# Kernel optimization log

Measured on AMD Instinct MI355X. Metric: run time of the kernel, lower is better.

Reference implementation:

```python
import jax, jax.numpy as jnp
import numpy as np

BSZ, SEQ, D, NHEAD, NLAYER, DFF, NQ = 4, 48, 256, 2, 2, 2048, 512
LN_EPS = 1e-5
NEG = jnp.float32(-1e30)


def _layernorm(x, w, b):
    m = jnp.mean(x, axis=-1, keepdims=True)
    v = jnp.mean((x - m) ** 2, axis=-1, keepdims=True)
    return (x - m) / jnp.sqrt(v + LN_EPS) * w + b


def _span_max(x):
    # Cumulative span max: span[b,s,e] = max(x[b,s:e+1]) for e>=s, else 0.
    B, S, H = x.shape
    padded = jnp.concatenate([x, jnp.full((B, S, H), NEG, x.dtype)], axis=1)  # [B,2S,H]

    def step(tmp, i):
        shifted = jax.lax.dynamic_slice(padded, (0, i, 0), (B, S, H))  # x shifted left by i, padded with -inf
        tmp = jnp.maximum(tmp, shifted)  # tmp[b,s] = max(x[b,s:s+i+1])
        return tmp, tmp

    _, ys = jax.lax.scan(step, jnp.full((B, S, H), NEG, x.dtype), jnp.arange(S))
    # ys: [width, B, start, H]; span[b,s,e] = ys[e-s, b, s]
    si = jnp.arange(S)[:, None]
    ei = jnp.arange(S)[None, :]
    w = jnp.clip(ei - si, 0, S - 1)
    span = ys[w, :, jnp.broadcast_to(si, (S, S))]  # [S_start, S_end, B, H]
    span = jnp.where((ei >= si)[:, :, None, None], span, 0.0)
    return span.transpose(2, 0, 1, 3)  # [B,S,S,H]


def _mha(x, wi, bi, wo, bo, kpm):
    # x: [B,T,D]; kpm: [B,T] bool, True = masked key
    B, T, Dm = x.shape
    hd = Dm // NHEAD
    qkv = x @ wi.T + bi
    q, k, v = jnp.split(qkv, 3, axis=-1)
    rs = lambda a: a.reshape(B, T, NHEAD, hd).transpose(0, 2, 1, 3)
    q, k, v = rs(q), rs(k), rs(v)
    scores = jnp.einsum('bhqd,bhkd->bhqk', q, k) * (1.0 / np.sqrt(hd))
    scores = jnp.where(kpm[:, None, None, :], -1e9, scores)
    p = jax.nn.softmax(scores, axis=-1)
    o = jnp.einsum('bhqk,bhkd->bhqd', p, v).transpose(0, 2, 1, 3).reshape(B, T, Dm)
    return o @ wo.T + bo


def _encoder(x, kpm, iw, ib, ow, ob, l1w, l1b, l2w, l2b, f1w, f1b, f2w, f2b, fw, fb):
    # Post-norm torch TransformerEncoder (eval mode, relu, no dropout)
    for l in range(NLAYER):
        a = _mha(x, iw[l], ib[l], ow[l], ob[l], kpm)
        x = _layernorm(x + a, l1w[l], l1b[l])
        f = jax.nn.relu(x @ f1w[l].T + f1b[l]) @ f2w[l].T + f2b[l]
        x = _layernorm(x + f, l2w[l], l2b[l])
    return _layernorm(x, fw, fb)


def _forward(enc, iw, ib, ow, ob, l1w, l1b, l2w, l2b, f1w, f1b, f2w, f2b, fw, fb, s1, e1, qb, s2, e2):
    span = _span_max(enc)  # [B,S,S,D]
    idx = jnp.arange(SEQ)
    kpm2d = idx[None, :] < idx[:, None]  # [start,end]: True where end < start
    kpm = jnp.broadcast_to(kpm2d.reshape(1, SEQ * SEQ), (BSZ, SEQ * SEQ))
    out = _encoder(span.reshape(BSZ, SEQ * SEQ, D), kpm, iw, ib, ow, ob, l1w, l1b, l2w, l2b, f1w, f1b, f2w, f2b, fw, fb)
    out = out.reshape(BSZ, SEQ, SEQ, D)
    res1 = out[qb, s1, e1]
    res2 = out[qb, s2, e2]
    return res1, res2


def setup_inputs() -> dict:
    key = jax.random.key(0)
    ks = jax.random.split(key, 16)
    sc = 0.02
    enc = jax.random.normal(ks[0], (BSZ, SEQ, D), jnp.float32)
    inp = {
        'encoded_input': enc,
        'in_proj_w': jax.random.normal(ks[1], (NLAYER, 3 * D, D), jnp.float32) * sc,
        'in_proj_b': jnp.zeros((NLAYER, 3 * D), jnp.float32),
        'out_proj_w': jax.random.normal(ks[2], (NLAYER, D, D), jnp.float32) * sc,
        'out_proj_b': jnp.zeros((NLAYER, D), jnp.float32),
        'ln1_w': jnp.ones((NLAYER, D), jnp.float32),
        'ln1_b': jnp.zeros((NLAYER, D), jnp.float32),
        'ln2_w': jnp.ones((NLAYER, D), jnp.float32),
        'ln2_b': jnp.zeros((NLAYER, D), jnp.float32),
        'ff1_w': jax.random.normal(ks[3], (NLAYER, DFF, D), jnp.float32) * sc,
        'ff1_b': jnp.zeros((NLAYER, DFF), jnp.float32),
        'ff2_w': jax.random.normal(ks[4], (NLAYER, D, DFF), jnp.float32) * sc,
        'ff2_b': jnp.zeros((NLAYER, D), jnp.float32),
        'fln_w': jnp.ones((D,), jnp.float32),
        'fln_b': jnp.zeros((D,), jnp.float32),
    }
    s1 = jax.random.randint(ks[5], (NQ,), 0, SEQ)
    e1 = jnp.minimum(s1 + jax.random.randint(ks[6], (NQ,), 0, SEQ), SEQ - 1)
    s2 = jax.random.randint(ks[7], (NQ,), 0, SEQ)
    e2 = jnp.minimum(s2 + jax.random.randint(ks[8], (NQ,), 0, SEQ), SEQ - 1)
    inp['start_ids_1'] = s1
    inp['end_ids_1'] = e1
    inp['query_batch_idx'] = jax.random.randint(ks[9], (NQ,), 0, BSZ)
    inp['start_ids_2'] = s2
    inp['end_ids_2'] = e2
    return inp


def reference(encoded_input, in_proj_w, in_proj_b, out_proj_w, out_proj_b, ln1_w, ln1_b, ln2_w, ln2_b, ff1_w, ff1_b, ff2_w, ff2_b, fln_w, fln_b, start_ids_1, end_ids_1, query_batch_idx, start_ids_2, end_ids_2):
    return _forward(encoded_input, in_proj_w, in_proj_b, out_proj_w, out_proj_b, ln1_w, ln1_b, ln2_w, ln2_b, ff1_w, ff1_b, ff2_w, ff2_b, fln_w, fln_b, start_ids_1, end_ids_1, query_batch_idx, start_ids_2, end_ids_2)
```

## Files before the change

### kernel.cpp

```cpp
#include <hip/hip_runtime.h>
#include <hip/hip_bf16.h>

#define BSZ 4
#define SEQ 48
#define DMODEL 256
#define NHEAD 2
#define HD 128
#define NLAYERS 2
#define DFF_C 2048
#define NQ_C 512
#define NV 1176
#define NTOT (BSZ * NV)
#define NVP 1216
#define KSPLIT 5
#define SCALE 0.088388347648318447f

typedef unsigned short u16;
typedef __attribute__((ext_vector_type(8))) short bf16x8;
typedef __attribute__((ext_vector_type(4))) float f32x4;

__device__ inline u16 f2b(float f) {
    __hip_bfloat16 h = __float2bfloat16(f);
    return *reinterpret_cast<u16*>(&h);
}
__device__ inline void storeval(float* p, float v) { *p = v; }
__device__ inline void storeval(u16* p, float v) { *p = f2b(v); }

__global__ __launch_bounds__(256) void span_kernel(const float* __restrict__ enc,
                                                   float* __restrict__ X,
                                                   u16* __restrict__ Xb) {
    int i = blockIdx.x, b = blockIdx.y, h = threadIdx.x;
    int tb = i * SEQ - (i * (i - 1)) / 2 - i;
    float run = -1e30f;
    for (int j = i; j < SEQ; ++j) {
        run = fmaxf(run, enc[((size_t)b * SEQ + j) * DMODEL + h]);
        size_t idx = ((size_t)b * NV + tb + j) * DMODEL + h;
        X[idx] = run;
        Xb[idx] = f2b(run);
    }
}

__global__ __launch_bounds__(256) void castall_kernel(
    const float* __restrict__ iw, const float* __restrict__ ow,
    const float* __restrict__ f1w, const float* __restrict__ f2w,
    u16* __restrict__ iwb, u16* __restrict__ owb,
    u16* __restrict__ f1wb, u16* __restrict__ f2wb) {
    int i = blockIdx.x * 256 + threadIdx.x;
    const float* src;
    u16* dst;
    int off;
    if (i < 98304)       { src = iw;  dst = iwb;  off = i; }
    else if (i < 131072) { src = ow;  dst = owb;  off = i - 98304; }
    else if (i < 393216) { src = f1w; dst = f1wb; off = i - 131072; }
    else                 { src = f2w; dst = f2wb; off = i - 393216; }
    float4 v = *(const float4*)(src + (size_t)off * 4);
    *(ushort4*)(dst + (size_t)off * 4) =
        make_ushort4(f2b(v.x), f2b(v.y), f2b(v.z), f2b(v.w));
}

template <typename OutT, bool RELU, bool ATOMIC>
__global__ __launch_bounds__(256) void mm_kernel(
    const u16* __restrict__ A, const u16* __restrict__ W,
    const float* __restrict__ bias, const float* __restrict__ Res,
    OutT* __restrict__ C, int N, int K, int lda, int ldw, int ldc,
    float alpha, int WV, int KC) {
    __shared__ u16 As[64][40];
    __shared__ u16 Ws[64][40];
    const float4 fz = make_float4(0.f, 0.f, 0.f, 0.f);
    int ks = blockIdx.z;
    int kb = ks * KC, ke = min(K, kb + KC);
    int p0 = blockIdx.x * 64, n0 = blockIdx.y * 64;
    int tid = threadIdx.x, lane = tid & 63, w = tid >> 6;
    int col_l = lane & 15, quad = lane >> 4;
    f32x4 acc[4] = {};
    for (int k0 = kb; k0 < ke; k0 += 32) {
        int r = tid >> 2, seg = (tid & 3) * 8;
        {
            int gn = n0 + r;
            float4 av = fz;
            if (gn < N) av = *(const float4*)(A + (size_t)gn * lda + k0 + seg);
            *(float4*)&As[r][seg] = av;
        }
        {
            int gp = p0 + r;
            float4 wv = fz;
            if (gp < WV) wv = *(const float4*)(W + (size_t)gp * ldw + k0 + seg);
            *(float4*)&Ws[r][seg] = wv;
        }
        __syncthreads();
        bf16x8 a = *(const bf16x8*)&As[w * 16 + col_l][quad * 8];
#pragma unroll
        for (int c = 0; c < 4; ++c) {
            bf16x8 b = *(const bf16x8*)&Ws[c * 16 + col_l][quad * 8];
            acc[c] = __builtin_amdgcn_mfma_f32_16x16x32_bf16(a, b, acc[c], 0, 0, 0);
        }
        __syncthreads();
    }
#pragma unroll
    for (int c = 0; c < 4; ++c) {
        int col = p0 + c * 16 + col_l;
        float bv = bias ? bias[col] : 0.f;
#pragma unroll
        for (int reg = 0; reg < 4; ++reg) {
            int row = n0 + w * 16 + quad * 4 + reg;
            if (row < N) {
                float v = acc[c][reg] * alpha + bv;
                if (Res) v += Res[(size_t)row * ldc + col];
                if (RELU) v = fmaxf(v, 0.f);
                if (ATOMIC) {
                    unsafeAtomicAdd((float*)&C[(size_t)row * ldc + col], v);
                } else {
                    storeval(&C[(size_t)row * ldc + col], v);
                }
            }
        }
    }
}

__global__ __launch_bounds__(256) void vtrans_kernel(const u16* __restrict__ QKVb,
                                                     u16* __restrict__ VT) {
    __shared__ u16 T[64][66];
    const float4 fz = make_float4(0.f, 0.f, 0.f, 0.f);
    int kt = blockIdx.x, dt = blockIdx.y, bh = blockIdx.z;
    int b = bh >> 1, h = bh & 1;
    size_t rb = (size_t)b * NV;
    int tid = threadIdx.x;
    {
        int r = tid >> 2, cs = (tid & 3) * 16;
        int key = kt * 64 + r;
        float4 v0 = fz, v1 = fz;
        if (key < NV) {
            const u16* vp = QKVb + (rb + key) * 768 + 2 * DMODEL + h * HD + dt * 64 + cs;
            v0 = *(const float4*)vp;
            v1 = *(const float4*)(vp + 8);
        }
        *(float4*)&T[r][cs] = v0;
        *(float4*)&T[r][cs + 8] = v1;
    }
    __syncthreads();
    {
        int dl = tid >> 2, ks2 = (tid & 3) * 16;
        u16 tmp[16];
#pragma unroll
        for (int j = 0; j < 16; ++j) tmp[j] = T[ks2 + j][dl];
        u16* dst = VT + ((size_t)bh * HD + dt * 64 + dl) * NVP + kt * 64 + ks2;
        *(float4*)dst = *(float4*)&tmp[0];
        *(float4*)(dst + 8) = *(float4*)&tmp[8];
    }
}

__global__ __launch_bounds__(256) void flash_kernel(const u16* __restrict__ QKVb,
                                                    const u16* __restrict__ VT,
                                                    float* __restrict__ Opart,
                                                    float* __restrict__ ML) {
    __shared__ u16 Ks[64][136];
    __shared__ u16 Vt[128][72];
    __shared__ u16 Ps[4][16][72];
    const float4 fz = make_float4(0.f, 0.f, 0.f, 0.f);
    int tid = threadIdx.x, lane = tid & 63, w = tid >> 6;
    int col_l = lane & 15, quad = lane >> 4;
    int bh = blockIdx.y, b = bh >> 1, h = bh & 1;
    int ks = blockIdx.z;
    int t0 = ks * 4, tcnt = min(4, 19 - t0);
    size_t rb = (size_t)b * NV;
    int q0 = blockIdx.x * 64, wq0 = q0 + w * 16;

    float4 qv[4];
    {
        int qrow = wq0 + col_l;
        if (qrow < NV) {
            const u16* qp = QKVb + (rb + qrow) * 768 + h * HD + quad * 8;
#pragma unroll
            for (int kf = 0; kf < 4; ++kf) qv[kf] = *(const float4*)(qp + kf * 32);
        } else {
#pragma unroll
            for (int kf = 0; kf < 4; ++kf) qv[kf] = fz;
        }
    }

    f32x4 oacc[8] = {};
    float m_run[4], l_run[4];
#pragma unroll
    for (int r = 0; r < 4; ++r) { m_run[r] = -1e30f; l_run[r] = 0.f; }

    for (int it = 0; it < tcnt; ++it) {
        int kt = (t0 + it) * 64;
        {
            int r = tid >> 2, seg = (tid & 3) * 32;
            int key = kt + r;
            const u16* kp = QKVb + (rb + key) * 768 + DMODEL + h * HD + seg;
#pragma unroll
            for (int t4 = 0; t4 < 4; ++t4) {
                float4 v = fz;
                if (key < NV) v = *(const float4*)(kp + t4 * 8);
                *(float4*)&Ks[r][seg + t4 * 8] = v;
            }
        }
        {
            int d = tid >> 1, half = (tid & 1) * 32;
            const u16* vp = VT + ((size_t)bh * HD + d) * NVP + kt + half;
#pragma unroll
            for (int t4 = 0; t4 < 4; ++t4)
                *(float4*)&Vt[d][half + t4 * 8] = *(const float4*)(vp + t4 * 8);
        }
        __syncthreads();

        f32x4 s[4] = {};
#pragma unroll
        for (int c = 0; c < 4; ++c)
#pragma unroll
            for (int kf = 0; kf < 4; ++kf) {
                bf16x8 kfr = *(const bf16x8*)&Ks[c * 16 + col_l][kf * 32 + quad * 8];
                s[c] = __builtin_amdgcn_mfma_f32_16x16x32_bf16(
                    *(const bf16x8*)&qv[kf], kfr, s[c], 0, 0, 0);
            }

        float pv[4][4];
#pragma unroll
        for (int c = 0; c < 4; ++c) {
            bool kvalid = (kt + c * 16 + col_l) < NV;
#pragma unroll
            for (int r = 0; r < 4; ++r)
                pv[c][r] = kvalid ? s[c][r] * SCALE : -1e30f;
        }
        float al[4];
#pragma unroll
        for (int r = 0; r < 4; ++r) {
            float mx = fmaxf(fmaxf(pv[0][r], pv[1][r]), fmaxf(pv[2][r], pv[3][r]));
#pragma unroll
            for (int off = 1; off < 16; off <<= 1)
                mx = fmaxf(mx, __shfl_xor(mx, off));
            float mn = fmaxf(m_run[r], mx);
            al[r] = __expf(m_run[r] - mn);
            m_run[r] = mn;
            float sum = 0.f;
#pragma unroll
            for (int c = 0; c < 4; ++c) {
                float p = __expf(pv[c][r] - mn);
                pv[c][r] = p;
                sum += p;
            }
#pragma unroll
            for (int off = 1; off < 16; off <<= 1) sum += __shfl_xor(sum, off);
            l_run[r] = l_run[r] * al[r] + sum;
        }
#pragma unroll
        for (int ct = 0; ct < 8; ++ct)
#pragma unroll
            for (int r = 0; r < 4; ++r) oacc[ct][r] *= al[r];

#pragma unroll
        for (int c = 0; c < 4; ++c)
#pragma unroll
            for (int r = 0; r < 4; ++r)
                Ps[w][quad * 4 + r][c * 16 + col_l] = f2b(pv[c][r]);
        bf16x8 pf0 = *(const bf16x8*)&Ps[w][col_l][quad * 8];
        bf16x8 pf1 = *(const bf16x8*)&Ps[w][col_l][32 + quad * 8];
#pragma unroll
        for (int ct = 0; ct < 8; ++ct) {
            bf16x8 v0 = *(const bf16x8*)&Vt[ct * 16 + col_l][quad * 8];
            bf16x8 v1 = *(const bf16x8*)&Vt[ct * 16 + col_l][32 + quad * 8];
            oacc[ct] = __builtin_amdgcn_mfma_f32_16x16x32_bf16(pf0, v0, oacc[ct], 0, 0, 0);
            oacc[ct] = __builtin_amdgcn_mfma_f32_16x16x32_bf16(pf1, v1, oacc[ct], 0, 0, 0);
        }
        __syncthreads();
    }

    size_t slab = (size_t)(ks * 8 + bh) * NVP;
#pragma unroll
    for (int ct = 0; ct < 8; ++ct)
#pragma unroll
        for (int r = 0; r < 4; ++r) {
            int row = wq0 + quad * 4 + r;
            Opart[(slab + row) * HD + ct * 16 + col_l] = oacc[ct][r];
        }
    if (col_l == 0) {
#pragma unroll
        for (int r = 0; r < 4; ++r) {
            int row = wq0 + quad * 4 + r;
            ML[(slab + row) * 2 + 0] = m_run[r];
            ML[(slab + row) * 2 + 1] = l_run[r];
        }
    }
}

__global__ __launch_bounds__(256) void comb_kernel(const float* __restrict__ Opart,
                                                   const float* __restrict__ ML,
                                                   u16* __restrict__ Obuf) {
    int bh = blockIdx.y, b = bh >> 1, h = bh & 1;
    int tid = threadIdx.x;
    int row = blockIdx.x * 2 + (tid >> 7);
    int d = tid & 127;
    if (row >= NV) return;
    float m[KSPLIT], l[KSPLIT];
#pragma unroll
    for (int i = 0; i < KSPLIT; ++i) {
        size_t mb = ((size_t)(i * 8 + bh) * NVP + row) * 2;
        m[i] = ML[mb];
        l[i] = ML[mb + 1];
    }
    float M = m[0];
#pragma unroll
    for (int i = 1; i < KSPLIT; ++i) M = fmaxf(M, m[i]);
    float wsum = 0.f, o = 0.f;
#pragma unroll
    for (int i = 0; i < KSPLIT; ++i) {
        float wi = __expf(m[i] - M);
        wsum += l[i] * wi;
        o += Opart[((size_t)(i * 8 + bh) * NVP + row) * HD + d] * wi;
    }
    Obuf[((size_t)b * NV + row) * DMODEL + h * HD + d] = f2b(o / wsum);
}

__global__ __launch_bounds__(256) void ln_kernel(const float* __restrict__ Xin,
                                                 const float* __restrict__ Res,
                                                 const float* __restrict__ w,
                                                 const float* __restrict__ bb,
                                                 float* __restrict__ Y,
                                                 u16* __restrict__ Yb,
                                                 const float* __restrict__ fb2,
                                                 float* __restrict__ A2out) {
    int r = blockIdx.x, d = threadIdx.x;
    size_t idx = (size_t)r * DMODEL + d;
    float v = Xin[idx];
    if (Res) v += Res[idx];
    float s1 = v, s2 = v * v;
#pragma unroll
    for (int off = 32; off > 0; off >>= 1) {
        s1 += __shfl_down(s1, off);
        s2 += __shfl_down(s2, off);
    }
    __shared__ float ps1[4], ps2[4];
    int wid = d >> 6, lane = d & 63;
    if (lane == 0) { ps1[wid] = s1; ps2[wid] = s2; }
    __syncthreads();
    if (d == 0) {
        ps1[0] = ps1[0] + ps1[1] + ps1[2] + ps1[3];
        ps2[0] = ps2[0] + ps2[1] + ps2[2] + ps2[3];
    }
    __syncthreads();
    float mean = ps1[0] * (1.f / DMODEL);
    float var = ps2[0] * (1.f / DMODEL) - mean * mean;
    float o = (v - mean) * rsqrtf(var + 1e-5f) * w[d] + bb[d];
    Y[idx] = o;
    Yb[idx] = f2b(o);
    if (A2out) A2out[idx] = o + fb2[d];
}

__global__ __launch_bounds__(256) void gather_kernel(const float* __restrict__ Xf,
                                                     const int* __restrict__ s1,
                                                     const int* __restrict__ e1,
                                                     const int* __restrict__ qb,
                                                     const int* __restrict__ s2,
                                                     const int* __restrict__ e2,
                                                     float* __restrict__ out) {
    int q = blockIdx.x, which = blockIdx.y, d = threadIdx.x;
    int s = which ? s2[q] : s1[q];
    int e = which ? e2[q] : e1[q];
    int b = qb[q];
    int t = s * SEQ - (s * (s - 1)) / 2 + (e - s);
    if (t < 0) t = 0;
    if (t >= NV) t = NV - 1;
    out[((size_t)which * NQ_C + q) * DMODEL + d] = Xf[((size_t)b * NV + t) * DMODEL + d];
}

extern "C" void kernel_launch(void* const* d_in, const int* in_sizes, int n_in,
                              void* d_out, int out_size, void* d_ws, size_t ws_size,
                              hipStream_t stream) {
    const float* enc = (const float*)d_in[0];
    const float* iw  = (const float*)d_in[1];
    const float* ib  = (const float*)d_in[2];
    const float* ow  = (const float*)d_in[3];
    const float* ob  = (const float*)d_in[4];
    const float* l1w = (const float*)d_in[5];
    const float* l1b = (const float*)d_in[6];
    const float* l2w = (const float*)d_in[7];
    const float* l2b = (const float*)d_in[8];
    const float* f1w = (const float*)d_in[9];
    const float* f1b = (const float*)d_in[10];
    const float* f2w = (const float*)d_in[11];
    const float* f2b_ = (const float*)d_in[12];
    const float* flw = (const float*)d_in[13];
    const float* flb = (const float*)d_in[14];
    const int* s1 = (const int*)d_in[15];
    const int* e1 = (const int*)d_in[16];
    const int* qb = (const int*)d_in[17];
    const int* s2 = (const int*)d_in[18];
    const int* e2 = (const int*)d_in[19];
    float* out = (float*)d_out;

    char* p = (char*)d_ws;
    float* X     = (float*)p;  p += (size_t)NTOT * DMODEL * 4;
    float* A2    = (float*)p;  p += (size_t)NTOT * DMODEL * 4;
    u16* Xb      = (u16*)p;    p += (size_t)NTOT * DMODEL * 2;
    u16* Obuf    = (u16*)p;    p += (size_t)NTOT * DMODEL * 2;
    u16* QKVb    = (u16*)p;    p += (size_t)NTOT * 3 * DMODEL * 2;
    u16* VT      = (u16*)p;    p += (size_t)8 * HD * NVP * 2;
    float* ML    = (float*)p;  p += (size_t)KSPLIT * 8 * NVP * 2 * 4;
    float* Opart = (float*)p;  p += (size_t)KSPLIT * 8 * NVP * HD * 4;
    u16* wb      = (u16*)p;
    u16* F1b     = (u16*)Opart;
    float* Of    = A2;

    u16* iwb  = wb;
    u16* owb  = iwb + 2 * 3 * DMODEL * DMODEL;
    u16* f1wb = owb + 2 * DMODEL * DMODEL;
    u16* f2wb = f1wb + 2 * DFF_C * DMODEL;

    castall_kernel<<<dim3(2560), 256, 0, stream>>>(iw, ow, f1w, f2w,
                                                   iwb, owb, f1wb, f2wb);
    span_kernel<<<dim3(SEQ, BSZ), 256, 0, stream>>>(enc, X, Xb);

    for (int l = 0; l < NLAYERS; ++l) {
        mm_kernel<u16, false, false><<<dim3(12, 74, 1), 256, 0, stream>>>(
            Xb, iwb + (size_t)l * 3 * DMODEL * DMODEL, ib + (size_t)l * 3 * DMODEL,
            nullptr, QKVb, NTOT, DMODEL, DMODEL, DMODEL, 3 * DMODEL, 1.f,
            3 * DMODEL, DMODEL);
        vtrans_kernel<<<dim3(19, 2, 8), 256, 0, stream>>>(QKVb, VT);
        flash_kernel<<<dim3(19, 8, KSPLIT), 256, 0, stream>>>(QKVb, VT, Opart, ML);
        comb_kernel<<<dim3(588, 8), 256, 0, stream>>>(Opart, ML, Obuf);
        mm_kernel<float, false, false><<<dim3(4, 74, 1), 256, 0, stream>>>(
            Obuf, owb + (size_t)l * DMODEL * DMODEL, ob + (size_t)l * DMODEL,
            X, A2, NTOT, DMODEL, DMODEL, DMODEL, DMODEL, 1.f, DMODEL, DMODEL);
        ln_kernel<<<dim3(NTOT), 256, 0, stream>>>(
            A2, nullptr, l1w + (size_t)l * DMODEL, l1b + (size_t)l * DMODEL,
            X, Xb, f2b_ + (size_t)l * DMODEL, A2);
        mm_kernel<u16, true, false><<<dim3(32, 74, 1), 256, 0, stream>>>(
            Xb, f1wb + (size_t)l * DFF_C * DMODEL, f1b + (size_t)l * DFF_C,
            nullptr, F1b, NTOT, DMODEL, DMODEL, DMODEL, DFF_C, 1.f, DFF_C, DMODEL);
        mm_kernel<float, false, true><<<dim3(4, 74, 4), 256, 0, stream>>>(
            F1b, f2wb + (size_t)l * DMODEL * DFF_C, nullptr, nullptr, A2,
            NTOT, DFF_C, DFF_C, DFF_C, DMODEL, 1.f, DMODEL, 512);
        ln_kernel<<<dim3(NTOT), 256, 0, stream>>>(
            A2, nullptr, l2w + (size_t)l * DMODEL, l2b + (size_t)l * DMODEL,
            X, Xb, nullptr, nullptr);
    }
    ln_kernel<<<dim3(NTOT), 256, 0, stream>>>(X, nullptr, flw, flb, Of, Xb,
                                              nullptr, nullptr);
    gather_kernel<<<dim3(NQ_C, 2), 256, 0, stream>>>(Of, s1, e1, qb, s2, e2, out);
}
```

Measured before the change: 360.5 us.

## Add 128x128-tile MFMA GEMM with direct global-to-LDS loads for QKV and FFN

Measured after the change: 376.7 us. +4.5%, slower.

```diff
diff --git a/kernel.cpp b/kernel.cpp
--- a/kernel.cpp
+++ b/kernel.cpp
@@ -11,6 +11,7 @@
 #define NQ_C 512
 #define NV 1176
 #define NTOT (BSZ * NV)
+#define NTOTP 4736
 #define NVP 1216
 #define KSPLIT 5
 #define SCALE 0.088388347648318447f
@@ -25,6 +26,12 @@
 }
 __device__ inline void storeval(float* p, float v) { *p = v; }
 __device__ inline void storeval(u16* p, float v) { *p = f2b(v); }
+
+__device__ inline void gload16(const u16* g, u16* l) {
+    __builtin_amdgcn_global_load_lds(
+        (__attribute__((address_space(1))) void*)(g),
+        (__attribute__((address_space(3))) void*)(l), 16, 0, 0);
+}
 
 __global__ __launch_bounds__(256) void span_kernel(const float* __restrict__ enc,
                                                    float* __restrict__ X,
@@ -111,6 +118,67 @@
                     unsafeAtomicAdd((float*)&C[(size_t)row * ldc + col], v);
                 } else {
                     storeval(&C[(size_t)row * ldc + col], v);
+                }
+            }
+        }
+    }
+}
+
+template <typename OutT, bool RELU, bool ATOMIC>
+__global__ __launch_bounds__(256) void mm128_kernel(
+    const u16* __restrict__ A, const u16* __restrict__ W,
+    const float* __restrict__ bias,
+    OutT* __restrict__ C, int N, int lda, int ldw, int ldc, int KC) {
+    __shared__ u16 As[128][32];
+    __shared__ u16 Ws[128][32];
+    int k0b = blockIdx.z * KC;
+    int p0 = blockIdx.x * 128, n0 = blockIdx.y * 128;
+    int tid = threadIdx.x, lane = tid & 63, w = tid >> 6;
+    int col_l = lane & 15, quad = lane >> 4;
+    int wr = w >> 1, wc = w & 1;
+    int ra = tid >> 2, ca = (tid & 3) * 8;
+    const u16* Abase = A + (size_t)(n0 + ra) * lda + ca;
+    const u16* Wbase = W + (size_t)(p0 + ra) * ldw + ca;
+    f32x4 acc[4][4] = {};
+    for (int kk = 0; kk < KC; kk += 32) {
+        int k0 = k0b + kk;
+        gload16(Abase + k0, &As[ra][ca]);
+        gload16(Abase + (size_t)64 * lda + k0, &As[64 + ra][ca]);
+        gload16(Wbase + k0, &Ws[ra][ca]);
+        gload16(Wbase + (size_t)64 * ldw + k0, &Ws[64 + ra][ca]);
+        __syncthreads();
+        bf16x8 a[4], b[4];
+#pragma unroll
+        for (int m = 0; m < 4; ++m)
+            a[m] = *(const bf16x8*)&As[wr * 64 + m * 16 + col_l][quad * 8];
+#pragma unroll
+        for (int c = 0; c < 4; ++c)
+            b[c] = *(const bf16x8*)&Ws[wc * 64 + c * 16 + col_l][quad * 8];
+#pragma unroll
+        for (int m = 0; m < 4; ++m)
+#pragma unroll
+            for (int c = 0; c < 4; ++c)
+                acc[m][c] = __builtin_amdgcn_mfma_f32_16x16x32_bf16(a[m], b[c],
+                                                                    acc[m][c], 0, 0, 0);
+        __syncthreads();
+    }
+#pragma unroll
+    for (int c = 0; c < 4; ++c) {
+        int col = p0 + wc * 64 + c * 16 + col_l;
+        float bv = bias ? bias[col] : 0.f;
+#pragma unroll
+        for (int m = 0; m < 4; ++m) {
+#pragma unroll
+            for (int reg = 0; reg < 4; ++reg) {
+                int row = n0 + wr * 64 + m * 16 + quad * 4 + reg;
+                if (row < N) {
+                    float v = acc[m][c][reg] + bv;
+                    if (RELU) v = fmaxf(v, 0.f);
+                    if (ATOMIC) {
+                        unsafeAtomicAdd((float*)&C[(size_t)row * ldc + col], v);
+                    } else {
+                        storeval(&C[(size_t)row * ldc + col], v);
+                    }
                 }
             }
         }
@@ -392,7 +460,7 @@
     char* p = (char*)d_ws;
     float* X     = (float*)p;  p += (size_t)NTOT * DMODEL * 4;
     float* A2    = (float*)p;  p += (size_t)NTOT * DMODEL * 4;
-    u16* Xb      = (u16*)p;    p += (size_t)NTOT * DMODEL * 2;
+    u16* Xb      = (u16*)p;    p += (size_t)NTOTP * DMODEL * 2;
     u16* Obuf    = (u16*)p;    p += (size_t)NTOT * DMODEL * 2;
     u16* QKVb    = (u16*)p;    p += (size_t)NTOT * 3 * DMODEL * 2;
     u16* VT      = (u16*)p;    p += (size_t)8 * HD * NVP * 2;
@@ -412,10 +480,9 @@
     span_kernel<<<dim3(SEQ, BSZ), 256, 0, stream>>>(enc, X, Xb);
 
     for (int l = 0; l < NLAYERS; ++l) {
-        mm_kernel<u16, false, false><<<dim3(12, 74, 1), 256, 0, stream>>>(
+        mm128_kernel<u16, false, false><<<dim3(6, 37, 1), 256, 0, stream>>>(
             Xb, iwb + (size_t)l * 3 * DMODEL * DMODEL, ib + (size_t)l * 3 * DMODEL,
-            nullptr, QKVb, NTOT, DMODEL, DMODEL, DMODEL, 3 * DMODEL, 1.f,
-            3 * DMODEL, DMODEL);
+            QKVb, NTOT, DMODEL, DMODEL, 3 * DMODEL, DMODEL);
         vtrans_kernel<<<dim3(19, 2, 8), 256, 0, stream>>>(QKVb, VT);
         flash_kernel<<<dim3(19, 8, KSPLIT), 256, 0, stream>>>(QKVb, VT, Opart, ML);
         comb_kernel<<<dim3(588, 8), 256, 0, stream>>>(Opart, ML, Obuf);
@@ -425,12 +492,12 @@
         ln_kernel<<<dim3(NTOT), 256, 0, stream>>>(
             A2, nullptr, l1w + (size_t)l * DMODEL, l1b + (size_t)l * DMODEL,
             X, Xb, f2b_ + (size_t)l * DMODEL, A2);
-        mm_kernel<u16, true, false><<<dim3(32, 74, 1), 256, 0, stream>>>(
+        mm128_kernel<u16, true, false><<<dim3(16, 37, 1), 256, 0, stream>>>(
             Xb, f1wb + (size_t)l * DFF_C * DMODEL, f1b + (size_t)l * DFF_C,
-            nullptr, F1b, NTOT, DMODEL, DMODEL, DMODEL, DFF_C, 1.f, DFF_C, DMODEL);
-        mm_kernel<float, false, true><<<dim3(4, 74, 4), 256, 0, stream>>>(
-            F1b, f2wb + (size_t)l * DMODEL * DFF_C, nullptr, nullptr, A2,
-            NTOT, DFF_C, DFF_C, DFF_C, DMODEL, 1.f, DMODEL, 512);
+            F1b, NTOT, DMODEL, DMODEL, DFF_C, DMODEL);
+        mm128_kernel<float, false, true><<<dim3(2, 37, 4), 256, 0, stream>>>(
+            F1b, f2wb + (size_t)l * DMODEL * DFF_C, nullptr, A2,
+            NTOT, DFF_C, DFF_C, DMODEL, 512);
         ln_kernel<<<dim3(NTOT), 256, 0, stream>>>(
             A2, nullptr, l2w + (size_t)l * DMODEL, l2b + (size_t)l * DMODEL,
             X, Xb, nullptr, nullptr);
```
